# Performance work log

Hardware: AMD Instinct MI355X
Metric: run time of the kernel (lower is better)

The kernel has to match this reference:

```python
import jax, jax.numpy as jnp
import numpy as np

E = 1024
H = 16
D = E // H
FF = 4 * E
EPS = 1e-5


def _layernorm(x, g, b):
    mu = jnp.mean(x, axis=-1, keepdims=True)
    var = jnp.mean(jnp.square(x - mu), axis=-1, keepdims=True)
    return (x - mu) * jax.lax.rsqrt(var + EPS) * g + b


def setup_inputs() -> dict:
    key = jax.random.key(0)
    ks = jax.random.split(key, 8)
    s_e = 1.0 / np.sqrt(E)
    s_f = 1.0 / np.sqrt(FF)
    return {
        "x": jax.random.normal(ks[0], (2, 2048, E), dtype=jnp.float32),
        "ln1_g": jnp.ones((E,), jnp.float32),
        "ln1_b": jnp.zeros((E,), jnp.float32),
        "qkv_w": jax.random.normal(ks[1], (E, 3 * E), jnp.float32) * s_e,
        "qkv_b": jnp.zeros((3 * E,), jnp.float32),
        "proj_w": jax.random.normal(ks[2], (E, E), jnp.float32) * s_e,
        "proj_b": jnp.zeros((E,), jnp.float32),
        "ln2_g": jnp.ones((E,), jnp.float32),
        "ln2_b": jnp.zeros((E,), jnp.float32),
        "fc1_w": jax.random.normal(ks[3], (E, FF), jnp.float32) * s_e,
        "fc1_b": jnp.zeros((FF,), jnp.float32),
        "fc2_w": jax.random.normal(ks[4], (FF, E), jnp.float32) * s_f,
        "fc2_b": jnp.zeros((E,), jnp.float32),
    }


def reference(x, ln1_g, ln1_b, qkv_w, qkv_b, proj_w, proj_b,
              ln2_g, ln2_b, fc1_w, fc1_b, fc2_w, fc2_b):
    B, N, _ = x.shape
    # --- pre-norm MHA ---
    h = _layernorm(x, ln1_g, ln1_b)
    qkv = (h @ qkv_w + qkv_b).reshape(B, N, 3, H, D)
    q, k, v = [jnp.moveaxis(qkv[:, :, i], 2, 1) for i in range(3)]  # [B,H,N,D]
    scores = jnp.einsum('bhnd,bhmd->bhnm', q, k) / np.sqrt(D)
    attn = jax.nn.softmax(scores, axis=-1)
    out = jnp.einsum('bhnm,bhmd->bnhd', attn, v).reshape(B, N, E)
    x = x + out @ proj_w + proj_b
    # --- pre-norm MLP ---
    h = _layernorm(x, ln2_g, ln2_b)
    h = jax.nn.gelu(h @ fc1_w + fc1_b, approximate=False)
    x = x + h @ fc2_w + fc2_b
    return x
```

## Files before the change

### kernel.cpp

```cpp
#include <hip/hip_runtime.h>
#include <hip/hip_bf16.h>
#include <math.h>

#define E_DIM 1024
#define NHEAD 16
#define HDIM 64
#define FF_DIM 4096
#define NBATCH 2
#define SEQLEN 2048
#define NTOK 4096
#define LN_EPS 1e-5f

typedef unsigned short bfu;
typedef __attribute__((ext_vector_type(8))) short bf16x8;
typedef __attribute__((ext_vector_type(4))) float f32x4;

static __device__ __forceinline__ bfu f2bf(float f) {
  __hip_bfloat16 h = __float2bfloat16(f);
  return *reinterpret_cast<bfu*>(&h);
}

static __device__ __forceinline__ void gld16(const bfu* g, bfu* l) {
  __builtin_amdgcn_global_load_lds(
      (const __attribute__((address_space(1))) void*)g,
      (__attribute__((address_space(3))) void*)l, 16, 0, 0);
}

__global__ __launch_bounds__(256) void transpose_cvt(
    const float* __restrict__ W, bfu* __restrict__ Wt, int R, int C) {
  __shared__ float t[32][33];
  int c0 = blockIdx.x * 32, r0 = blockIdx.y * 32;
#pragma unroll
  for (int i = 0; i < 32; i += 8)
    t[threadIdx.y + i][threadIdx.x] =
        W[(size_t)(r0 + threadIdx.y + i) * C + c0 + threadIdx.x];
  __syncthreads();
#pragma unroll
  for (int i = 0; i < 32; i += 8)
    Wt[(size_t)(c0 + threadIdx.y + i) * R + r0 + threadIdx.x] =
        f2bf(t[threadIdx.x][threadIdx.y + i]);
}

__global__ __launch_bounds__(256) void ln_kernel(
    const float* __restrict__ x, const float* __restrict__ g,
    const float* __restrict__ b, bfu* __restrict__ out) {
  int row = blockIdx.x;
  float4 v = reinterpret_cast<const float4*>(x + (size_t)row * E_DIM)[threadIdx.x];
  float s = v.x + v.y + v.z + v.w;
  float s2 = v.x * v.x + v.y * v.y + v.z * v.z + v.w * v.w;
#pragma unroll
  for (int off = 1; off < 64; off <<= 1) {
    s += __shfl_xor(s, off);
    s2 += __shfl_xor(s2, off);
  }
  __shared__ float red[8];
  int wv = threadIdx.x >> 6;
  if ((threadIdx.x & 63) == 0) { red[wv] = s; red[4 + wv] = s2; }
  __syncthreads();
  s = red[0] + red[1] + red[2] + red[3];
  s2 = red[4] + red[5] + red[6] + red[7];
  float mu = s * (1.f / E_DIM);
  float var = s2 * (1.f / E_DIM) - mu * mu;
  float rs = rsqrtf(var + LN_EPS);
  int c = threadIdx.x * 4;
  ushort4 o;
  o.x = f2bf((v.x - mu) * rs * g[c + 0] + b[c + 0]);
  o.y = f2bf((v.y - mu) * rs * g[c + 1] + b[c + 1]);
  o.z = f2bf((v.z - mu) * rs * g[c + 2] + b[c + 2]);
  o.w = f2bf((v.w - mu) * rs * g[c + 3] + b[c + 3]);
  reinterpret_cast<ushort4*>(out + (size_t)row * E_DIM)[threadIdx.x] = o;
}

template <int EP, int BN>
__global__ __launch_bounds__(256) void gemm_kernel(
    const bfu* __restrict__ A, const bfu* __restrict__ Bt,
    int M, int N, int K,
    const float* __restrict__ bias, const float* __restrict__ resid,
    float* __restrict__ outf, bfu* __restrict__ outb,
    bfu* __restrict__ qo, bfu* __restrict__ ko, bfu* __restrict__ vo) {
  constexpr int NJ = BN / 32;
  __shared__ __align__(16) bfu As[2][128][64];
  __shared__ __align__(16) bfu Bs[2][BN][64];
  const int tid = threadIdx.x;
  const int lane = tid & 63, wv = tid >> 6;
  const int wr = (wv >> 1) * 64, wc = (wv & 1) * (BN / 2);
  const int gx = gridDim.x, nwg = gx * gridDim.y;
  const int hw = blockIdx.y * gx + blockIdx.x;
  const int lg = (hw & 7) * (nwg >> 3) + (hw >> 3);
  const int m0 = (lg / gx) * 128, n0 = (lg % gx) * BN;

  f32x4 acc[4][NJ];
#pragma unroll
  for (int i = 0; i < 4; i++)
#pragma unroll
    for (int j = 0; j < NJ; j++) acc[i][j] = (f32x4){0.f, 0.f, 0.f, 0.f};

  const int sr = lane >> 3;
  const int scs = ((lane & 7) ^ (sr & 7)) * 8;
  const int rsw = (lane & 7) << 3;

  auto stage = [&](int buf, int k0) {
#pragma unroll
    for (int c = 0; c < 4; c++) {
      int r = wv * 32 + c * 8;
      gld16(A + (size_t)(m0 + r + sr) * K + k0 + scs, &As[buf][r][0]);
    }
#pragma unroll
    for (int c = 0; c < BN / 32; c++) {
      int r = wv * (BN / 4) + c * 8;
      gld16(Bt + (size_t)(n0 + r + sr) * K + k0 + scs, &Bs[buf][r][0]);
    }
  };

  stage(0, 0);
  __syncthreads();
  const int NT = K >> 6;
  int cur = 0;
  for (int t = 0; t < NT; t++) {
    if (t + 1 < NT) stage(cur ^ 1, (t + 1) * 64);
#pragma unroll
    for (int kk = 0; kk < 2; kk++) {
      const int ce = (kk * 32 + (lane >> 4) * 8) ^ rsw;
      bf16x8 af[4], bfr[NJ];
#pragma unroll
      for (int i = 0; i < 4; i++)
        af[i] = *reinterpret_cast<const bf16x8*>(&As[cur][wr + i * 16 + (lane & 15)][ce]);
#pragma unroll
      for (int j = 0; j < NJ; j++)
        bfr[j] = *reinterpret_cast<const bf16x8*>(&Bs[cur][wc + j * 16 + (lane & 15)][ce]);
#pragma unroll
      for (int i = 0; i < 4; i++)
#pragma unroll
        for (int j = 0; j < NJ; j++)
          acc[i][j] = __builtin_amdgcn_mfma_f32_16x16x32_bf16(af[i], bfr[j], acc[i][j], 0, 0, 0);
    }
    __syncthreads();
    cur ^= 1;
  }

  const int cr = (lane >> 4) * 4, cc = lane & 15;
#pragma unroll
  for (int i = 0; i < 4; i++) {
#pragma unroll
    for (int j = 0; j < NJ; j++) {
      const int gn = n0 + wc + j * 16 + cc;
      const float bb = bias[gn];
#pragma unroll
      for (int r = 0; r < 4; r++) {
        const int gm = m0 + wr + i * 16 + cr + r;
        float val = acc[i][j][r] + bb;
        if (EP == 0) {
          int which = gn >> 10, rem = gn & 1023;
          int hh = rem >> 6, dd = rem & 63;
          int b_ = gm >> 11, nn = gm & 2047;
          size_t dst = (((size_t)(b_ * NHEAD + hh)) * SEQLEN + nn) * HDIM + dd;
          if (which == 0) qo[dst] = f2bf(val * 0.125f);
          else if (which == 1) ko[dst] = f2bf(val);
          else vo[dst] = f2bf(val);
        } else if (EP == 1) {
          outf[(size_t)gm * N + gn] = val + resid[(size_t)gm * N + gn];
        } else if (EP == 2) {
          outb[(size_t)gm * N + gn] = f2bf(0.5f * val * (1.f + erff(val * 0.70710678f)));
        } else {
          outf[(size_t)gm * N + gn] = val + resid[(size_t)gm * N + gn];
        }
      }
    }
  }
}

__global__ __launch_bounds__(256) void attn_kernel(
    const bfu* __restrict__ q, const bfu* __restrict__ kbuf,
    const bfu* __restrict__ vbuf, bfu* __restrict__ o) {
  __shared__ __align__(16) bfu Ks[64][64];
  __shared__ __align__(16) bfu Vt[64][72];
  __shared__ __align__(16) bfu Ps[4][16][72];

  const int hw = blockIdx.y * gridDim.x + blockIdx.x;
  const int lg = (hw & 7) * 128 + (hw >> 3);
  const int bh = lg >> 5;
  const int q0 = (lg & 31) * 64;
  const int tid = threadIdx.x, lane = tid & 63, wv = tid >> 6;
  const size_t base = (size_t)bh * SEQLEN * HDIM;
  const bfu* qp = q + base;
  const bfu* kp = kbuf + base;
  const bfu* vp = vbuf + base;

  const int qr = q0 + wv * 16 + (lane & 15);
  bf16x8 qf[2];
  qf[0] = *reinterpret_cast<const bf16x8*>(qp + (size_t)qr * HDIM + (lane >> 4) * 8);
  qf[1] = *reinterpret_cast<const bf16x8*>(qp + (size_t)qr * HDIM + 32 + (lane >> 4) * 8);

  float mrun = -1e30f, lrun = 0.f;
  f32x4 oacc[4];
#pragma unroll
  for (int d = 0; d < 4; d++) oacc[d] = (f32x4){0.f, 0.f, 0.f, 0.f};

  const int sr = lane >> 3;
  const int scs = ((lane & 7) ^ (sr & 7)) * 8;
  const int vrow = tid & 63, vcb = (tid >> 6) * 16;

  for (int kt = 0; kt < SEQLEN; kt += 64) {
#pragma unroll
    for (int c = 0; c < 2; c++) {
      int ch = wv * 2 + c;
      gld16(kp + (size_t)(kt + ch * 8 + sr) * HDIM + scs, &Ks[ch * 8][0]);
    }
    bf16x8 v0 = *reinterpret_cast<const bf16x8*>(vp + (size_t)(kt + vrow) * HDIM + vcb);
    bf16x8 v1 = *reinterpret_cast<const bf16x8*>(vp + (size_t)(kt + vrow) * HDIM + vcb + 8);
#pragma unroll
    for (int j = 0; j < 8; j++) {
      Vt[vcb + j][vrow] = (bfu)(unsigned short)v0[j];
      Vt[vcb + 8 + j][vrow] = (bfu)(unsigned short)v1[j];
    }
    __syncthreads();

    f32x4 st[4];
    __builtin_amdgcn_s_setprio(1);
#pragma unroll
    for (int kc = 0; kc < 4; kc++) {
      f32x4 a = (f32x4){0.f, 0.f, 0.f, 0.f};
#pragma unroll
      for (int kk = 0; kk < 2; kk++) {
        int ce = (kk * 32 + (lane >> 4) * 8) ^ ((lane & 7) << 3);
        bf16x8 kf = *reinterpret_cast<const bf16x8*>(&Ks[kc * 16 + (lane & 15)][ce]);
        a = __builtin_amdgcn_mfma_f32_16x16x32_bf16(kf, qf[kk], a, 0, 0, 0);
      }
      st[kc] = a;
    }
    __builtin_amdgcn_s_setprio(0);

    float t0 = fmaxf(fmaxf(st[0][0], st[0][1]), fmaxf(st[0][2], st[0][3]));
    float t1 = fmaxf(fmaxf(st[1][0], st[1][1]), fmaxf(st[1][2], st[1][3]));
    float t2 = fmaxf(fmaxf(st[2][0], st[2][1]), fmaxf(st[2][2], st[2][3]));
    float t3 = fmaxf(fmaxf(st[3][0], st[3][1]), fmaxf(st[3][2], st[3][3]));
    float t = fmaxf(fmaxf(t0, t1), fmaxf(t2, t3));
    t = fmaxf(t, __shfl_xor(t, 16));
    t = fmaxf(t, __shfl_xor(t, 32));

    bool resc = t > mrun + 8.f;
    if (__any(resc)) {
      float alpha = resc ? __expf(mrun - t) : 1.f;
      if (resc) mrun = t;
      lrun *= alpha;
#pragma unroll
      for (int r = 0; r < 4; r++) {
        float ar = __shfl(alpha, (lane >> 4) * 4 + r);
#pragma unroll
        for (int d = 0; d < 4; d++) oacc[d][r] *= ar;
      }
    }

    float p[4][4], ps = 0.f;
#pragma unroll
    for (int kc = 0; kc < 4; kc++)
#pragma unroll
      for (int r = 0; r < 4; r++) {
        p[kc][r] = __expf(st[kc][r] - mrun);
        ps += p[kc][r];
      }
    ps += __shfl_xor(ps, 16);
    ps += __shfl_xor(ps, 32);
    lrun += ps;

    const int qcol = lane & 15, g4 = (lane >> 4) * 4;
#pragma unroll
    for (int kc = 0; kc < 4; kc++) {
      ushort4 pk;
      pk.x = f2bf(p[kc][0]); pk.y = f2bf(p[kc][1]);
      pk.z = f2bf(p[kc][2]); pk.w = f2bf(p[kc][3]);
      *reinterpret_cast<ushort4*>(&Ps[wv][qcol][kc * 16 + g4]) = pk;
    }

    bf16x8 pf[2];
#pragma unroll
    for (int ks = 0; ks < 2; ks++)
      pf[ks] = *reinterpret_cast<const bf16x8*>(
          &Ps[wv][lane & 15][ks * 32 + (lane >> 4) * 8]);
    __builtin_amdgcn_s_setprio(1);
#pragma unroll
    for (int d = 0; d < 4; d++) {
#pragma unroll
      for (int ks = 0; ks < 2; ks++) {
        bf16x8 vf = *reinterpret_cast<const bf16x8*>(
            &Vt[d * 16 + (lane & 15)][ks * 32 + (lane >> 4) * 8]);
        oacc[d] = __builtin_amdgcn_mfma_f32_16x16x32_bf16(pf[ks], vf, oacc[d], 0, 0, 0);
      }
    }
    __builtin_amdgcn_s_setprio(0);
    __syncthreads();
  }

  int b_ = bh >> 4, hh = bh & 15;
#pragma unroll
  for (int r = 0; r < 4; r++) {
    float lr = __shfl(lrun, (lane >> 4) * 4 + r);
    float rl = 1.f / lr;
#pragma unroll
    for (int d = 0; d < 4; d++) {
      int row = q0 + wv * 16 + (lane >> 4) * 4 + r;
      int col = hh * HDIM + d * 16 + (lane & 15);
      o[((size_t)(b_ * SEQLEN + row)) * E_DIM + col] = f2bf(oacc[d][r] * rl);
    }
  }
}

extern "C" void kernel_launch(void* const* d_in, const int* in_sizes, int n_in,
                              void* d_out, int out_size, void* d_ws, size_t ws_size,
                              hipStream_t stream) {
  (void)in_sizes; (void)n_in; (void)out_size; (void)ws_size;
  const float* x      = (const float*)d_in[0];
  const float* ln1_g  = (const float*)d_in[1];
  const float* ln1_b  = (const float*)d_in[2];
  const float* qkv_w  = (const float*)d_in[3];
  const float* qkv_b  = (const float*)d_in[4];
  const float* proj_w = (const float*)d_in[5];
  const float* proj_b = (const float*)d_in[6];
  const float* ln2_g  = (const float*)d_in[7];
  const float* ln2_b  = (const float*)d_in[8];
  const float* fc1_w  = (const float*)d_in[9];
  const float* fc1_b  = (const float*)d_in[10];
  const float* fc2_w  = (const float*)d_in[11];
  const float* fc2_b  = (const float*)d_in[12];
  float* out = (float*)d_out;

  char* p = (char*)d_ws;
  auto carve = [&](size_t n) { char* r = p; p += (n + 255) & ~(size_t)255; return r; };
  bfu* qkv_wt  = (bfu*)carve((size_t)3 * E_DIM * E_DIM * 2);
  bfu* proj_wt = (bfu*)carve((size_t)E_DIM * E_DIM * 2);
  bfu* fc1_wt  = (bfu*)carve((size_t)FF_DIM * E_DIM * 2);
  bfu* fc2_wt  = (bfu*)carve((size_t)E_DIM * FF_DIM * 2);
  bfu* hbuf    = (bfu*)carve((size_t)NTOK * E_DIM * 2);
  bfu* region  = (bfu*)carve((size_t)NTOK * FF_DIM * 2);
  float* x1    = (float*)carve((size_t)NTOK * E_DIM * 4);
  bfu* qb = region;
  bfu* kb = region + (size_t)NTOK * E_DIM;
  bfu* vb = region + (size_t)2 * NTOK * E_DIM;
  bfu* ao = region + (size_t)3 * NTOK * E_DIM;
  bfu* h3 = region;

  dim3 tb(32, 8);
  transpose_cvt<<<dim3(3 * E_DIM / 32, E_DIM / 32), tb, 0, stream>>>(qkv_w, qkv_wt, E_DIM, 3 * E_DIM);
  transpose_cvt<<<dim3(E_DIM / 32, E_DIM / 32), tb, 0, stream>>>(proj_w, proj_wt, E_DIM, E_DIM);
  transpose_cvt<<<dim3(FF_DIM / 32, E_DIM / 32), tb, 0, stream>>>(fc1_w, fc1_wt, E_DIM, FF_DIM);
  transpose_cvt<<<dim3(E_DIM / 32, FF_DIM / 32), tb, 0, stream>>>(fc2_w, fc2_wt, FF_DIM, E_DIM);

  ln_kernel<<<NTOK, 256, 0, stream>>>(x, ln1_g, ln1_b, hbuf);
  gemm_kernel<0, 128><<<dim3(3 * E_DIM / 128, NTOK / 128), 256, 0, stream>>>(
      hbuf, qkv_wt, NTOK, 3 * E_DIM, E_DIM, qkv_b, nullptr, nullptr, nullptr, qb, kb, vb);
  attn_kernel<<<dim3(SEQLEN / 64, NBATCH * NHEAD), 256, 0, stream>>>(qb, kb, vb, ao);
  gemm_kernel<1, 64><<<dim3(E_DIM / 64, NTOK / 128), 256, 0, stream>>>(
      ao, proj_wt, NTOK, E_DIM, E_DIM, proj_b, x, x1, nullptr, nullptr, nullptr, nullptr);
  ln_kernel<<<NTOK, 256, 0, stream>>>(x1, ln2_g, ln2_b, hbuf);
  gemm_kernel<2, 128><<<dim3(FF_DIM / 128, NTOK / 128), 256, 0, stream>>>(
      hbuf, fc1_wt, NTOK, FF_DIM, E_DIM, fc1_b, nullptr, nullptr, h3, nullptr, nullptr, nullptr);
  gemm_kernel<3, 64><<<dim3(E_DIM / 64, NTOK / 128), 256, 0, stream>>>(
      h3, fc2_wt, NTOK, E_DIM, FF_DIM, fc2_b, x1, out, nullptr, nullptr, nullptr, nullptr);
}
```

Before: 359.7 us.

## Double-buffer K/V tiles in attention kernel to overlap loads with compute

Attention K and V shared-memory tiles become double-buffered. The next tile's K async LDS load and V register loads are issued before the current tile's QK^T/softmax/PV work, and V is transposed into the alternate buffer afterward, leaving one barrier per iteration. This targets global-load latency that was exposed on every key tile, at the cost of twice the K/V LDS footprint and more live registers, which could lower occupancy.

```diff
diff --git a/kernel.cpp b/kernel.cpp
--- a/kernel.cpp
+++ b/kernel.cpp
@@ -172,8 +172,8 @@
 __global__ __launch_bounds__(256) void attn_kernel(
     const bfu* __restrict__ q, const bfu* __restrict__ kbuf,
     const bfu* __restrict__ vbuf, bfu* __restrict__ o) {
-  __shared__ __align__(16) bfu Ks[64][64];
-  __shared__ __align__(16) bfu Vt[64][72];
+  __shared__ __align__(16) bfu Ks[2][64][64];
+  __shared__ __align__(16) bfu Vt[2][64][72];
   __shared__ __align__(16) bfu Ps[4][16][72];
 
   const int hw = blockIdx.y * gridDim.x + blockIdx.x;
@@ -200,20 +200,37 @@
   const int scs = ((lane & 7) ^ (sr & 7)) * 8;
   const int vrow = tid & 63, vcb = (tid >> 6) * 16;
 
-  for (int kt = 0; kt < SEQLEN; kt += 64) {
-#pragma unroll
-    for (int c = 0; c < 2; c++) {
-      int ch = wv * 2 + c;
-      gld16(kp + (size_t)(kt + ch * 8 + sr) * HDIM + scs, &Ks[ch * 8][0]);
-    }
-    bf16x8 v0 = *reinterpret_cast<const bf16x8*>(vp + (size_t)(kt + vrow) * HDIM + vcb);
-    bf16x8 v1 = *reinterpret_cast<const bf16x8*>(vp + (size_t)(kt + vrow) * HDIM + vcb + 8);
+#pragma unroll
+  for (int c = 0; c < 2; c++) {
+    int ch = wv * 2 + c;
+    gld16(kp + (size_t)(ch * 8 + sr) * HDIM + scs, &Ks[0][ch * 8][0]);
+  }
+  {
+    bf16x8 v0 = *reinterpret_cast<const bf16x8*>(vp + (size_t)vrow * HDIM + vcb);
+    bf16x8 v1 = *reinterpret_cast<const bf16x8*>(vp + (size_t)vrow * HDIM + vcb + 8);
 #pragma unroll
     for (int j = 0; j < 8; j++) {
-      Vt[vcb + j][vrow] = (bfu)(unsigned short)v0[j];
-      Vt[vcb + 8 + j][vrow] = (bfu)(unsigned short)v1[j];
-    }
-    __syncthreads();
+      Vt[0][vcb + j][vrow] = (bfu)(unsigned short)v0[j];
+      Vt[0][vcb + 8 + j][vrow] = (bfu)(unsigned short)v1[j];
+    }
+  }
+  __syncthreads();
+
+  const int NT = SEQLEN / 64;
+  for (int t = 0; t < NT; t++) {
+    const int cur = t & 1, nxt = cur ^ 1;
+    const bool pre = (t + 1 < NT);
+    bf16x8 nv0, nv1;
+    if (pre) {
+      const int kn = (t + 1) * 64;
+#pragma unroll
+      for (int c = 0; c < 2; c++) {
+        int ch = wv * 2 + c;
+        gld16(kp + (size_t)(kn + ch * 8 + sr) * HDIM + scs, &Ks[nxt][ch * 8][0]);
+      }
+      nv0 = *reinterpret_cast<const bf16x8*>(vp + (size_t)(kn + vrow) * HDIM + vcb);
+      nv1 = *reinterpret_cast<const bf16x8*>(vp + (size_t)(kn + vrow) * HDIM + vcb + 8);
+    }
 
     f32x4 st[4];
     __builtin_amdgcn_s_setprio(1);
@@ -223,7 +240,7 @@
 #pragma unroll
       for (int kk = 0; kk < 2; kk++) {
         int ce = (kk * 32 + (lane >> 4) * 8) ^ ((lane & 7) << 3);
-        bf16x8 kf = *reinterpret_cast<const bf16x8*>(&Ks[kc * 16 + (lane & 15)][ce]);
+        bf16x8 kf = *reinterpret_cast<const bf16x8*>(&Ks[cur][kc * 16 + (lane & 15)][ce]);
         a = __builtin_amdgcn_mfma_f32_16x16x32_bf16(kf, qf[kk], a, 0, 0, 0);
       }
       st[kc] = a;
@@ -234,14 +251,14 @@
     float t1 = fmaxf(fmaxf(st[1][0], st[1][1]), fmaxf(st[1][2], st[1][3]));
     float t2 = fmaxf(fmaxf(st[2][0], st[2][1]), fmaxf(st[2][2], st[2][3]));
     float t3 = fmaxf(fmaxf(st[3][0], st[3][1]), fmaxf(st[3][2], st[3][3]));
-    float t = fmaxf(fmaxf(t0, t1), fmaxf(t2, t3));
-    t = fmaxf(t, __shfl_xor(t, 16));
-    t = fmaxf(t, __shfl_xor(t, 32));
-
-    bool resc = t > mrun + 8.f;
+    float tm = fmaxf(fmaxf(t0, t1), fmaxf(t2, t3));
+    tm = fmaxf(tm, __shfl_xor(tm, 16));
+    tm = fmaxf(tm, __shfl_xor(tm, 32));
+
+    bool resc = tm > mrun + 8.f;
     if (__any(resc)) {
-      float alpha = resc ? __expf(mrun - t) : 1.f;
-      if (resc) mrun = t;
+      float alpha = resc ? __expf(mrun - tm) : 1.f;
+      if (resc) mrun = tm;
       lrun *= alpha;
 #pragma unroll
       for (int r = 0; r < 4; r++) {
@@ -283,11 +300,19 @@
 #pragma unroll
       for (int ks = 0; ks < 2; ks++) {
         bf16x8 vf = *reinterpret_cast<const bf16x8*>(
-            &Vt[d * 16 + (lane & 15)][ks * 32 + (lane >> 4) * 8]);
+            &Vt[cur][d * 16 + (lane & 15)][ks * 32 + (lane >> 4) * 8]);
         oacc[d] = __builtin_amdgcn_mfma_f32_16x16x32_bf16(pf[ks], vf, oacc[d], 0, 0, 0);
       }
     }
     __builtin_amdgcn_s_setprio(0);
+
+    if (pre) {
+#pragma unroll
+      for (int j = 0; j < 8; j++) {
+        Vt[nxt][vcb + j][vrow] = (bfu)(unsigned short)nv0[j];
+        Vt[nxt][vcb + 8 + j][vrow] = (bfu)(unsigned short)nv1[j];
+      }
+    }
     __syncthreads();
   }
 
```

New measurement: 390.6 us. 1.09x slower.
